# Kernel tuning notes

Hardware: AMD Instinct MI355X
Metric: run time of the kernel (lower is better)

The kernel has to match this reference:

```python
import jax, jax.numpy as jnp
import numpy as np

B, R, C, IN, OUT = 64, 4608, 32, 8, 16


def squash(s, axis=-1):
    sq = jnp.sum(s * s, axis=axis, keepdims=True)
    return (sq / (1.0 + sq)) * s / jnp.sqrt(sq + 1e-8)


def setup_inputs() -> dict:
    key = jax.random.key(0)
    k1, k2 = jax.random.split(key)
    x = jax.random.normal(k1, (B, R, IN), dtype=jnp.float32)
    route_weights = jax.random.normal(k2, (R, C, IN, OUT), dtype=jnp.float32)
    return {"x": x, "route_weights": route_weights}


def reference(x, route_weights):
    # u_hat: (B, C, R, OUT) -- predictions from each route to each capsule
    u_hat = jnp.einsum('bri,rcio->bcro', x, route_weights)
    b = jnp.zeros((B, C, R, 1), dtype=u_hat.dtype)
    v = None
    for _ in range(3):  # fixed 3 routing iterations
        c = jax.nn.softmax(b, axis=2)           # over capsules dim=2 (matches torch dim=2)
        s = jnp.sum(c * u_hat, axis=2)          # (B, C, OUT)
        v = squash(s)                           # (B, C, OUT)
        b = b + jnp.sum(u_hat * v[:, :, None, :], axis=-1, keepdims=True)
    return v
```

## Files before the change

kernel.cpp:

```cpp
#include <hip/hip_runtime.h>
#include <cmath>

#define BB 64
#define RR 4608
#define CC 32
#define INN 8
#define OUTT 16

constexpr int RC = 24;
constexpr int NCHUNK = RR / RC;
constexpr int CT = 4;
constexpr int XS_STRIDE = RC * INN + 4;

__global__ __launch_bounds__(256, 3)
void caps_pass(const float* __restrict__ x, const float* __restrict__ W,
               const float* __restrict__ V, float* __restrict__ pz,
               float* __restrict__ ps)
{
    __shared__ float xs[BB][XS_STRIDE];

    const int tid  = threadIdx.x;
    const int lane = tid & 63;
    const int wv   = tid >> 6;
    const int ch   = blockIdx.x;
    const int r0   = ch * RC;
    const int c    = __builtin_amdgcn_readfirstlane(blockIdx.y * CT + wv);

    {
        const int F4_PER_B = (RC * INN) / 4;
        const int T4 = BB * F4_PER_B;
        for (int t4 = tid; t4 < T4; t4 += 256) {
            int b = t4 / F4_PER_B;
            int j = t4 % F4_PER_B;
            float4 v = *reinterpret_cast<const float4*>(
                x + ((size_t)b * RR + r0) * INN + 4 * j);
            *reinterpret_cast<float4*>(&xs[b][4 * j]) = v;
        }
    }
    __syncthreads();

    float Vr[OUTT];
    {
        const float* vp = V + ((size_t)c * BB + lane) * OUTT;
#pragma unroll
        for (int o = 0; o < OUTT; ++o) Vr[o] = vp[o];
    }

    float z = 0.f;
    float sacc[OUTT];
#pragma unroll
    for (int o = 0; o < OUTT; ++o) sacc[o] = 0.f;

    for (int r = 0; r < RC; ++r) {
        float4 xA = *reinterpret_cast<const float4*>(&xs[lane][r * INN]);
        float4 xB = *reinterpret_cast<const float4*>(&xs[lane][r * INN + 4]);
        float xi[INN] = { xA.x, xA.y, xA.z, xA.w, xB.x, xB.y, xB.z, xB.w };

        const float* Wr = W + (((size_t)(r0 + r) * CC + c) * INN) * OUTT;

        float uh[OUTT];
#pragma unroll
        for (int o = 0; o < OUTT; ++o) uh[o] = 0.f;
#pragma unroll
        for (int i = 0; i < INN; ++i) {
#pragma unroll
            for (int o = 0; o < OUTT; ++o)
                uh[o] = fmaf(xi[i], Wr[i * OUTT + o], uh[o]);
        }

        float logit = 0.f;
#pragma unroll
        for (int o = 0; o < OUTT; ++o) logit = fmaf(uh[o], Vr[o], logit);

        float p = __expf(logit);
        z += p;
#pragma unroll
        for (int o = 0; o < OUTT; ++o) sacc[o] = fmaf(p, uh[o], sacc[o]);
    }

    const size_t base = ((size_t)ch * CC + c) * BB + lane;
    pz[base] = z;
    float* psp = ps + base * OUTT;
#pragma unroll
    for (int q = 0; q < OUTT / 4; ++q) {
        float4 v4 = make_float4(sacc[4 * q], sacc[4 * q + 1],
                                sacc[4 * q + 2], sacc[4 * q + 3]);
        *reinterpret_cast<float4*>(psp + 4 * q) = v4;
    }
}

template <int LAST>
__global__ __launch_bounds__(256)
void caps_combine(const float* __restrict__ pz, const float* __restrict__ ps,
                  float* __restrict__ V, float* __restrict__ out)
{
    const int tid = blockIdx.x * 256 + threadIdx.x;
    const int o  = tid & 15;
    const int bc = tid >> 4;
    const int b  = bc & 63;
    const int c  = bc >> 6;

    float Z = 0.f, sv = 0.f;
    for (int ch = 0; ch < NCHUNK; ++ch) {
        const size_t base = ((size_t)ch * CC + c) * BB + b;
        Z  += pz[base];
        sv += ps[base * OUTT + o];
    }
    float st = sv / Z;

    float sq = st * st;
#pragma unroll
    for (int m = 1; m < 16; m <<= 1) sq += __shfl_xor(sq, m);
    float scale = (sq / (1.0f + sq)) / sqrtf(sq + 1e-8f);
    float v = st * scale;

    if (LAST) {
        out[((size_t)b * CC + c) * OUTT + o] = v;
    } else {
        V[((size_t)c * BB + b) * OUTT + o] += v;
    }
}

extern "C" void kernel_launch(void* const* d_in, const int* in_sizes, int n_in,
                              void* d_out, int out_size, void* d_ws, size_t ws_size,
                              hipStream_t stream)
{
    const float* x = (const float*)d_in[0];
    const float* W = (const float*)d_in[1];
    float* out = (float*)d_out;

    float* wsf = (float*)d_ws;
    float* V  = wsf;
    float* pz = wsf + (size_t)BB * CC * OUTT;
    float* ps = pz + (size_t)NCHUNK * CC * BB;

    hipMemsetAsync(V, 0, (size_t)BB * CC * OUTT * sizeof(float), stream);

    dim3 grid(NCHUNK, CC / CT);
    for (int it = 0; it < 3; ++it) {
        caps_pass<<<grid, 256, 0, stream>>>(x, W, V, pz, ps);
        if (it < 2)
            caps_combine<0><<<128, 256, 0, stream>>>(pz, ps, V, out);
        else
            caps_combine<1><<<128, 256, 0, stream>>>(pz, ps, V, out);
    }
}
```

Baseline: 373.5 us.

## Double-buffer x staging in LDS with register prefetch and raise occupancy

Each block's 24-route slice of x is now staged in three 8-route pieces through two LDS buffers. The next piece is loaded into registers while the current one is computed, then written to the other buffer. This shrinks LDS per block, so launch bounds move to 4 waves per SIMD, and the global load latency of x should overlap with the FMA work. The combine loop also gets unroll 4. The risks are added syncthreads per stage and register pressure from holding the prefetch registers, which could cause spills at the higher occupancy target.

```diff
diff --git a/kernel.cpp b/kernel.cpp
--- a/kernel.cpp
+++ b/kernel.cpp
@@ -7,37 +7,50 @@
 #define INN 8
 #define OUTT 16
 
-constexpr int RC = 24;
-constexpr int NCHUNK = RR / RC;
-constexpr int CT = 4;
-constexpr int XS_STRIDE = RC * INN + 4;
+constexpr int RSTAGE = 8;
+constexpr int KCH    = 3;
+constexpr int RCB    = RSTAGE * KCH;
+constexpr int NCHUNK = RR / RCB;
+constexpr int CT     = 4;
+constexpr int XSTR   = RSTAGE * INN + 4;
 
-__global__ __launch_bounds__(256, 3)
+__global__ __launch_bounds__(256, 4)
 void caps_pass(const float* __restrict__ x, const float* __restrict__ W,
                const float* __restrict__ V, float* __restrict__ pz,
                float* __restrict__ ps)
 {
-    __shared__ float xs[BB][XS_STRIDE];
+    __shared__ float xs[2][BB][XSTR];
 
     const int tid  = threadIdx.x;
     const int lane = tid & 63;
     const int wv   = tid >> 6;
     const int ch   = blockIdx.x;
-    const int r0   = ch * RC;
+    const int r0   = ch * RCB;
     const int c    = __builtin_amdgcn_readfirstlane(blockIdx.y * CT + wv);
 
-    {
-        const int F4_PER_B = (RC * INN) / 4;
-        const int T4 = BB * F4_PER_B;
-        for (int t4 = tid; t4 < T4; t4 += 256) {
-            int b = t4 / F4_PER_B;
-            int j = t4 % F4_PER_B;
-            float4 v = *reinterpret_cast<const float4*>(
-                x + ((size_t)b * RR + r0) * INN + 4 * j);
-            *reinterpret_cast<float4*>(&xs[b][4 * j]) = v;
+    const int bq  = tid >> 4;
+    const int pos = tid & 15;
+
+    float4 st[4];
+
+    auto load_stage = [&](int rs) {
+#pragma unroll
+        for (int j = 0; j < 4; ++j) {
+            int b = j * 16 + bq;
+            st[j] = *reinterpret_cast<const float4*>(
+                x + ((size_t)b * RR + rs) * INN + pos * 4);
         }
-    }
-    __syncthreads();
+    };
+    auto write_stage = [&](int buf) {
+#pragma unroll
+        for (int j = 0; j < 4; ++j) {
+            int b = j * 16 + bq;
+            *reinterpret_cast<float4*>(&xs[buf][b][pos * 4]) = st[j];
+        }
+    };
+
+    load_stage(r0);
+    write_stage(0);
 
     float Vr[OUTT];
     {
@@ -51,31 +64,54 @@
 #pragma unroll
     for (int o = 0; o < OUTT; ++o) sacc[o] = 0.f;
 
-    for (int r = 0; r < RC; ++r) {
-        float4 xA = *reinterpret_cast<const float4*>(&xs[lane][r * INN]);
-        float4 xB = *reinterpret_cast<const float4*>(&xs[lane][r * INN + 4]);
-        float xi[INN] = { xA.x, xA.y, xA.z, xA.w, xB.x, xB.y, xB.z, xB.w };
+    __syncthreads();
 
-        const float* Wr = W + (((size_t)(r0 + r) * CC + c) * INN) * OUTT;
+    for (int k = 0; k < KCH; ++k) {
+        const int cur = k & 1;
 
-        float uh[OUTT];
+        if (k + 1 < KCH) load_stage(r0 + (k + 1) * RSTAGE);
+
+        const float* Wr = W + (((size_t)(r0 + k * RSTAGE) * CC + c) * INN) * OUTT;
+
+#pragma unroll 2
+        for (int r = 0; r < RSTAGE; ++r) {
+            float4 xA = *reinterpret_cast<const float4*>(&xs[cur][lane][r * INN]);
+            float4 xB = *reinterpret_cast<const float4*>(&xs[cur][lane][r * INN + 4]);
+
+            float uh[OUTT];
 #pragma unroll
-        for (int o = 0; o < OUTT; ++o) uh[o] = 0.f;
+            for (int o = 0; o < OUTT; ++o) uh[o] = 0.f;
 #pragma unroll
-        for (int i = 0; i < INN; ++i) {
+            for (int o = 0; o < OUTT; ++o) uh[o] = fmaf(xA.x, Wr[0 * OUTT + o], uh[o]);
 #pragma unroll
-            for (int o = 0; o < OUTT; ++o)
-                uh[o] = fmaf(xi[i], Wr[i * OUTT + o], uh[o]);
+            for (int o = 0; o < OUTT; ++o) uh[o] = fmaf(xA.y, Wr[1 * OUTT + o], uh[o]);
+#pragma unroll
+            for (int o = 0; o < OUTT; ++o) uh[o] = fmaf(xA.z, Wr[2 * OUTT + o], uh[o]);
+#pragma unroll
+            for (int o = 0; o < OUTT; ++o) uh[o] = fmaf(xA.w, Wr[3 * OUTT + o], uh[o]);
+#pragma unroll
+            for (int o = 0; o < OUTT; ++o) uh[o] = fmaf(xB.x, Wr[4 * OUTT + o], uh[o]);
+#pragma unroll
+            for (int o = 0; o < OUTT; ++o) uh[o] = fmaf(xB.y, Wr[5 * OUTT + o], uh[o]);
+#pragma unroll
+            for (int o = 0; o < OUTT; ++o) uh[o] = fmaf(xB.z, Wr[6 * OUTT + o], uh[o]);
+#pragma unroll
+            for (int o = 0; o < OUTT; ++o) uh[o] = fmaf(xB.w, Wr[7 * OUTT + o], uh[o]);
+
+            float logit = 0.f;
+#pragma unroll
+            for (int o = 0; o < OUTT; ++o) logit = fmaf(uh[o], Vr[o], logit);
+
+            float p = __expf(logit);
+            z += p;
+#pragma unroll
+            for (int o = 0; o < OUTT; ++o) sacc[o] = fmaf(p, uh[o], sacc[o]);
+
+            Wr += CC * INN * OUTT;
         }
 
-        float logit = 0.f;
-#pragma unroll
-        for (int o = 0; o < OUTT; ++o) logit = fmaf(uh[o], Vr[o], logit);
-
-        float p = __expf(logit);
-        z += p;
-#pragma unroll
-        for (int o = 0; o < OUTT; ++o) sacc[o] = fmaf(p, uh[o], sacc[o]);
+        if (k + 1 < KCH) write_stage(cur ^ 1);
+        __syncthreads();
     }
 
     const size_t base = ((size_t)ch * CC + c) * BB + lane;
@@ -101,8 +137,9 @@
     const int c  = bc >> 6;
 
     float Z = 0.f, sv = 0.f;
-    for (int ch = 0; ch < NCHUNK; ++ch) {
-        const size_t base = ((size_t)ch * CC + c) * BB + b;
+#pragma unroll 4
+    for (int chk = 0; chk < NCHUNK; ++chk) {
+        const size_t base = ((size_t)chk * CC + c) * BB + b;
         Z  += pz[base];
         sv += ps[base * OUTT + o];
     }
```

Measured after the change: 469.4 us. +25.7%, slower.

## Restructure capsule pass into 64-thread blocks and split chunk reduction in two stages

Applied to the files above, without the earlier changes.

The pass kernel now uses single-wave blocks in which each lane handles two batch rows for one of two capsules. It drops the shared-memory staging of x, reads x directly from global memory, and loads W as float4 so each weight is reused for two batch rows. The combine step is split into a grouped partial reduction over chunk groups followed by a small finish kernel, so the long serial 192-chunk loop is spread across more threads. The cost is an extra launch per iteration and uncached direct x loads, which are redundant across capsule blocks.

```diff
diff --git a/kernel.cpp b/kernel.cpp
--- a/kernel.cpp
+++ b/kernel.cpp
@@ -7,118 +7,174 @@
 #define INN 8
 #define OUTT 16
 
-constexpr int RC = 24;
-constexpr int NCHUNK = RR / RC;
-constexpr int CT = 4;
-constexpr int XS_STRIDE = RC * INN + 4;
-
-__global__ __launch_bounds__(256, 3)
+constexpr int RCB    = 24;
+constexpr int NCHUNK = RR / RCB;
+constexpr int NCQ    = CC / 2;
+constexpr int NG     = 8;
+constexpr int CPG    = NCHUNK / NG;
+
+__global__ __launch_bounds__(64, 3)
 void caps_pass(const float* __restrict__ x, const float* __restrict__ W,
                const float* __restrict__ V, float* __restrict__ pz,
                float* __restrict__ ps)
 {
-    __shared__ float xs[BB][XS_STRIDE];
-
-    const int tid  = threadIdx.x;
-    const int lane = tid & 63;
-    const int wv   = tid >> 6;
-    const int ch   = blockIdx.x;
-    const int r0   = ch * RC;
-    const int c    = __builtin_amdgcn_readfirstlane(blockIdx.y * CT + wv);
-
+    const int lane = threadIdx.x;
+    const int chh  = lane >> 5;
+    const int bs   = lane & 31;
+    const int cq   = blockIdx.x;
+    const int ch   = blockIdx.y;
+    const int c    = cq * 2 + chh;
+    const int r0   = ch * RCB;
+
+    float Vr0[OUTT], Vr1[OUTT];
     {
-        const int F4_PER_B = (RC * INN) / 4;
-        const int T4 = BB * F4_PER_B;
-        for (int t4 = tid; t4 < T4; t4 += 256) {
-            int b = t4 / F4_PER_B;
-            int j = t4 % F4_PER_B;
-            float4 v = *reinterpret_cast<const float4*>(
-                x + ((size_t)b * RR + r0) * INN + 4 * j);
-            *reinterpret_cast<float4*>(&xs[b][4 * j]) = v;
-        }
-    }
-    __syncthreads();
-
-    float Vr[OUTT];
-    {
-        const float* vp = V + ((size_t)c * BB + lane) * OUTT;
-#pragma unroll
-        for (int o = 0; o < OUTT; ++o) Vr[o] = vp[o];
-    }
-
-    float z = 0.f;
-    float sacc[OUTT];
-#pragma unroll
-    for (int o = 0; o < OUTT; ++o) sacc[o] = 0.f;
-
-    for (int r = 0; r < RC; ++r) {
-        float4 xA = *reinterpret_cast<const float4*>(&xs[lane][r * INN]);
-        float4 xB = *reinterpret_cast<const float4*>(&xs[lane][r * INN + 4]);
-        float xi[INN] = { xA.x, xA.y, xA.z, xA.w, xB.x, xB.y, xB.z, xB.w };
-
-        const float* Wr = W + (((size_t)(r0 + r) * CC + c) * INN) * OUTT;
-
-        float uh[OUTT];
-#pragma unroll
-        for (int o = 0; o < OUTT; ++o) uh[o] = 0.f;
+        const float* vp0 = V + ((size_t)c * BB + bs) * OUTT;
+        const float* vp1 = V + ((size_t)c * BB + bs + 32) * OUTT;
+#pragma unroll
+        for (int q = 0; q < 4; ++q) {
+            float4 a = *reinterpret_cast<const float4*>(vp0 + 4 * q);
+            float4 b = *reinterpret_cast<const float4*>(vp1 + 4 * q);
+            Vr0[4*q]=a.x; Vr0[4*q+1]=a.y; Vr0[4*q+2]=a.z; Vr0[4*q+3]=a.w;
+            Vr1[4*q]=b.x; Vr1[4*q+1]=b.y; Vr1[4*q+2]=b.z; Vr1[4*q+3]=b.w;
+        }
+    }
+
+    float z0 = 0.f, z1 = 0.f;
+    float s0[OUTT], s1[OUTT];
+#pragma unroll
+    for (int o = 0; o < OUTT; ++o) { s0[o] = 0.f; s1[o] = 0.f; }
+
+    const float* Wp  = W + ((size_t)r0 * CC + c) * (INN * OUTT);
+    const float* xp0 = x + ((size_t)bs * RR + r0) * INN;
+    const float* xp1 = x + ((size_t)(bs + 32) * RR + r0) * INN;
+
+    for (int r = 0; r < RCB; ++r) {
+        float4 xa0 = *reinterpret_cast<const float4*>(xp0 + r * INN);
+        float4 xb0 = *reinterpret_cast<const float4*>(xp0 + r * INN + 4);
+        float4 xa1 = *reinterpret_cast<const float4*>(xp1 + r * INN);
+        float4 xb1 = *reinterpret_cast<const float4*>(xp1 + r * INN + 4);
+        const float x0v[INN] = {xa0.x,xa0.y,xa0.z,xa0.w, xb0.x,xb0.y,xb0.z,xb0.w};
+        const float x1v[INN] = {xa1.x,xa1.y,xa1.z,xa1.w, xb1.x,xb1.y,xb1.z,xb1.w};
+
+        float uh0[OUTT], uh1[OUTT];
+#pragma unroll
+        for (int o = 0; o < OUTT; ++o) { uh0[o] = 0.f; uh1[o] = 0.f; }
+
+        const float4* W4 = reinterpret_cast<const float4*>(Wp);
 #pragma unroll
         for (int i = 0; i < INN; ++i) {
-#pragma unroll
-            for (int o = 0; o < OUTT; ++o)
-                uh[o] = fmaf(xi[i], Wr[i * OUTT + o], uh[o]);
-        }
-
-        float logit = 0.f;
-#pragma unroll
-        for (int o = 0; o < OUTT; ++o) logit = fmaf(uh[o], Vr[o], logit);
-
-        float p = __expf(logit);
-        z += p;
-#pragma unroll
-        for (int o = 0; o < OUTT; ++o) sacc[o] = fmaf(p, uh[o], sacc[o]);
-    }
-
-    const size_t base = ((size_t)ch * CC + c) * BB + lane;
-    pz[base] = z;
-    float* psp = ps + base * OUTT;
-#pragma unroll
-    for (int q = 0; q < OUTT / 4; ++q) {
-        float4 v4 = make_float4(sacc[4 * q], sacc[4 * q + 1],
-                                sacc[4 * q + 2], sacc[4 * q + 3]);
-        *reinterpret_cast<float4*>(psp + 4 * q) = v4;
-    }
+            const float xi0 = x0v[i];
+            const float xi1 = x1v[i];
+#pragma unroll
+            for (int q = 0; q < 4; ++q) {
+                const float4 w = W4[i * 4 + q];
+                uh0[q*4+0] = fmaf(xi0, w.x, uh0[q*4+0]);
+                uh0[q*4+1] = fmaf(xi0, w.y, uh0[q*4+1]);
+                uh0[q*4+2] = fmaf(xi0, w.z, uh0[q*4+2]);
+                uh0[q*4+3] = fmaf(xi0, w.w, uh0[q*4+3]);
+                uh1[q*4+0] = fmaf(xi1, w.x, uh1[q*4+0]);
+                uh1[q*4+1] = fmaf(xi1, w.y, uh1[q*4+1]);
+                uh1[q*4+2] = fmaf(xi1, w.z, uh1[q*4+2]);
+                uh1[q*4+3] = fmaf(xi1, w.w, uh1[q*4+3]);
+            }
+        }
+
+        float a0=0.f,a1=0.f,a2=0.f,a3=0.f, b0=0.f,b1=0.f,b2=0.f,b3=0.f;
+#pragma unroll
+        for (int q = 0; q < 4; ++q) {
+            a0 = fmaf(uh0[q],      Vr0[q],      a0);
+            a1 = fmaf(uh0[4 + q],  Vr0[4 + q],  a1);
+            a2 = fmaf(uh0[8 + q],  Vr0[8 + q],  a2);
+            a3 = fmaf(uh0[12 + q], Vr0[12 + q], a3);
+            b0 = fmaf(uh1[q],      Vr1[q],      b0);
+            b1 = fmaf(uh1[4 + q],  Vr1[4 + q],  b1);
+            b2 = fmaf(uh1[8 + q],  Vr1[8 + q],  b2);
+            b3 = fmaf(uh1[12 + q], Vr1[12 + q], b3);
+        }
+        const float p0 = __expf((a0 + a1) + (a2 + a3));
+        const float p1 = __expf((b0 + b1) + (b2 + b3));
+        z0 += p0;
+        z1 += p1;
+#pragma unroll
+        for (int o = 0; o < OUTT; ++o) {
+            s0[o] = fmaf(p0, uh0[o], s0[o]);
+            s1[o] = fmaf(p1, uh1[o], s1[o]);
+        }
+
+        Wp += CC * INN * OUTT;
+    }
+
+    const size_t bc0 = ((size_t)ch * CC + c) * BB + bs;
+    const size_t bc1 = bc0 + 32;
+    pz[bc0] = z0;
+    pz[bc1] = z1;
+    float* p0p = ps + bc0 * OUTT;
+    float* p1p = ps + bc1 * OUTT;
+#pragma unroll
+    for (int q = 0; q < 4; ++q) {
+        *reinterpret_cast<float4*>(p0p + 4*q) =
+            make_float4(s0[4*q], s0[4*q+1], s0[4*q+2], s0[4*q+3]);
+        *reinterpret_cast<float4*>(p1p + 4*q) =
+            make_float4(s1[4*q], s1[4*q+1], s1[4*q+2], s1[4*q+3]);
+    }
+}
+
+__global__ __launch_bounds__(256)
+void caps_reduce1(const float* __restrict__ pz, const float* __restrict__ ps,
+                  float* __restrict__ mz, float* __restrict__ ms)
+{
+    const int g    = blockIdx.y;
+    const int flat = blockIdx.x * 256 + threadIdx.x;
+    const int o    = flat & 15;
+    const int bc   = flat >> 4;
+    const int b    = bc & 63;
+    const int c    = bc >> 6;
+
+    float sv = 0.f;
+#pragma unroll 4
+    for (int j = 0; j < CPG; ++j) {
+        const size_t chk = (size_t)g * CPG + j;
+        sv += ps[(((chk * CC + c) * BB + b) << 4) + o];
+    }
+    float zv = 0.f;
+    for (int j = o; j < CPG; j += 16) {
+        const size_t chk = (size_t)g * CPG + j;
+        zv += pz[(chk * CC + c) * BB + b];
+    }
+#pragma unroll
+    for (int m = 1; m < 16; m <<= 1) zv += __shfl_xor(zv, m);
+
+    ms[(size_t)g * 32768 + flat] = sv;
+    if (o == 0) mz[(size_t)g * 2048 + bc] = zv;
 }
 
 template <int LAST>
 __global__ __launch_bounds__(256)
-void caps_combine(const float* __restrict__ pz, const float* __restrict__ ps,
-                  float* __restrict__ V, float* __restrict__ out)
-{
-    const int tid = blockIdx.x * 256 + threadIdx.x;
-    const int o  = tid & 15;
-    const int bc = tid >> 4;
-    const int b  = bc & 63;
-    const int c  = bc >> 6;
-
-    float Z = 0.f, sv = 0.f;
-    for (int ch = 0; ch < NCHUNK; ++ch) {
-        const size_t base = ((size_t)ch * CC + c) * BB + b;
-        Z  += pz[base];
-        sv += ps[base * OUTT + o];
-    }
-    float st = sv / Z;
+void caps_finish(const float* __restrict__ mz, const float* __restrict__ ms,
+                 float* __restrict__ V, float* __restrict__ out)
+{
+    const int flat = blockIdx.x * 256 + threadIdx.x;
+    const int o    = flat & 15;
+    const int bc   = flat >> 4;
+    const int b    = bc & 63;
+    const int c    = bc >> 6;
+
+    float sv = 0.f, zv = 0.f;
+#pragma unroll
+    for (int g = 0; g < NG; ++g) {
+        sv += ms[(size_t)g * 32768 + flat];
+        zv += mz[(size_t)g * 2048 + bc];
+    }
+    const float st = sv / zv;
 
     float sq = st * st;
 #pragma unroll
     for (int m = 1; m < 16; m <<= 1) sq += __shfl_xor(sq, m);
-    float scale = (sq / (1.0f + sq)) / sqrtf(sq + 1e-8f);
-    float v = st * scale;
-
-    if (LAST) {
-        out[((size_t)b * CC + c) * OUTT + o] = v;
-    } else {
-        V[((size_t)c * BB + b) * OUTT + o] += v;
-    }
+    const float scale = (sq / (1.0f + sq)) / sqrtf(sq + 1e-8f);
+    const float v = st * scale;
+
+    if (LAST) out[((size_t)b * CC + c) * OUTT + o] = v;
+    else      V[flat] += v;
 }
 
 extern "C" void kernel_launch(void* const* d_in, const int* in_sizes, int n_in,
@@ -131,17 +187,21 @@
 
     float* wsf = (float*)d_ws;
     float* V  = wsf;
-    float* pz = wsf + (size_t)BB * CC * OUTT;
+    float* pz = V  + (size_t)BB * CC * OUTT;
     float* ps = pz + (size_t)NCHUNK * CC * BB;
+    float* mz = ps + (size_t)NCHUNK * CC * BB * OUTT;
+    float* ms = mz + (size_t)NG * CC * BB;
 
     hipMemsetAsync(V, 0, (size_t)BB * CC * OUTT * sizeof(float), stream);
 
-    dim3 grid(NCHUNK, CC / CT);
+    const dim3 pgrid(NCQ, NCHUNK);
+    const dim3 rgrid(128, NG);
     for (int it = 0; it < 3; ++it) {
-        caps_pass<<<grid, 256, 0, stream>>>(x, W, V, pz, ps);
+        caps_pass<<<pgrid, 64, 0, stream>>>(x, W, V, pz, ps);
+        caps_reduce1<<<rgrid, 256, 0, stream>>>(pz, ps, mz, ms);
         if (it < 2)
-            caps_combine<0><<<128, 256, 0, stream>>>(pz, ps, V, out);
+            caps_finish<0><<<128, 256, 0, stream>>>(mz, ms, V, out);
         else
-            caps_combine<1><<<128, 256, 0, stream>>>(pz, ps, V, out);
-    }
-}
+            caps_finish<1><<<128, 256, 0, stream>>>(mz, ms, V, out);
+    }
+}
```

New measurement: 623.9 us. 1.67x slower.
